# Kernel optimization log

Hardware: AMD Instinct MI355X
Metric: run time of the kernel (lower is better)

Reference implementation:

```python
import jax, jax.numpy as jnp
import numpy as np

D = 128  # input_dim

def setup_inputs() -> dict:
    key = jax.random.key(0)
    ks = jax.random.split(key, 9)
    B, Lq, Lkv = 4, 4096, 4096
    s = 1.0 / np.sqrt(D)
    return {
        "x1": jax.random.normal(ks[0], (B, Lq, D), dtype=jnp.float32),
        "x2": jax.random.normal(ks[1], (B, Lkv, D), dtype=jnp.float32),
        "x3": jax.random.normal(ks[2], (B, Lkv, D), dtype=jnp.float32),
        "Wq": jax.random.normal(ks[3], (D, D), dtype=jnp.float32) * s,
        "bq": jax.random.normal(ks[4], (D,), dtype=jnp.float32) * s,
        "Wk": jax.random.normal(ks[5], (D, D), dtype=jnp.float32) * s,
        "bk": jax.random.normal(ks[6], (D,), dtype=jnp.float32) * s,
        "Wv": jax.random.normal(ks[7], (D, D), dtype=jnp.float32) * s,
        "bv": jax.random.normal(ks[8], (D,), dtype=jnp.float32) * s,
    }

def reference(x1, x2, x3, Wq, bq, Wk, bk, Wv, bv):
    # torch Linear: y = x @ W.T + b
    q = jnp.einsum('bld,ed->ble', x1, Wq) + bq  # [B,Lq,D]
    k = jnp.einsum('bld,ed->ble', x2, Wk) + bk  # [B,Lkv,D]
    v = jnp.einsum('bld,ed->ble', x3, Wv) + bv  # [B,Lkv,D]
    scores = jnp.einsum('bqd,bkd->bqk', q, k) / jnp.sqrt(jnp.float32(x1.shape[-1]))
    attn = jax.nn.softmax(scores, axis=2)
    return jnp.einsum('bqk,bkd->bqd', attn, v)
```

## Files before the change

### kernel.cpp

```cpp
#include <hip/hip_runtime.h>
#include <hip/hip_bf16.h>

typedef __attribute__((ext_vector_type(8))) short short8;
typedef __attribute__((ext_vector_type(4))) float v4f;
typedef __attribute__((ext_vector_type(4))) unsigned int uint4v;

__device__ __forceinline__ unsigned short f2bf(float f) {
    union { float f; unsigned u; } c; c.f = f;
    unsigned r = c.u + 0x7FFFu + ((c.u >> 16) & 1u);
    return (unsigned short)(r >> 16);
}
__device__ __forceinline__ unsigned pack2(float a, float b) {
    return (unsigned)f2bf(a) | ((unsigned)f2bf(b) << 16);
}
__device__ __forceinline__ float bf2f(unsigned short h) {
    union { unsigned u; float f; } c; c.u = ((unsigned)h) << 16;
    return c.f;
}

__device__ __forceinline__ void g2l16(const unsigned short* g, unsigned short* l) {
    __builtin_amdgcn_global_load_lds(
        (const __attribute__((address_space(1))) unsigned int*)g,
        (__attribute__((address_space(3))) unsigned int*)l,
        16, 0, 0);
}

__global__ __launch_bounds__(512) void proj_kernel(
    const float* __restrict__ x1, const float* __restrict__ x2, const float* __restrict__ x3,
    const float* __restrict__ Wq, const float* __restrict__ bq,
    const float* __restrict__ Wk, const float* __restrict__ bk,
    const float* __restrict__ Wv, const float* __restrict__ bv,
    unsigned short* __restrict__ qb, unsigned short* __restrict__ kb,
    unsigned short* __restrict__ vb, float qscale)
{
    __shared__ __attribute__((aligned(16))) unsigned short Smem[32768];
    unsigned short* Xs = Smem;
    unsigned short* Ws = Smem + 16384;
    unsigned short* Os = Smem;

    int tid = threadIdx.x;
    int wave = tid >> 6, lane = tid & 63;
    int lmod = lane & 15, ldiv = lane >> 4;
    int p = blockIdx.x % 3;
    int row0 = (blockIdx.x / 3) * 128;

    const float* X = p == 0 ? x1 : p == 1 ? x2 : x3;
    const float* W = p == 0 ? Wq : p == 1 ? Wk : Wv;
    const float* bias = p == 0 ? bq : p == 1 ? bk : bv;
    float scale = p == 0 ? qscale : 1.0f;

#pragma unroll
    for (int i = 0; i < 8; i++) {
        int c = tid + i * 512;
        int row = c >> 5, d0 = (c & 31) * 4;
        v4f f = *(const v4f*)(X + (size_t)(row0 + row) * 128 + d0);
        int off = ((row >> 4) * 16 + (d0 >> 5) * 4 + ((d0 >> 3) & 3)) * 128 + (row & 15) * 8 + (d0 & 7);
        *(uint2*)&Xs[off] = make_uint2(pack2(f[0], f[1]), pack2(f[2], f[3]));
        v4f g = *(const v4f*)(W + (size_t)row * 128 + d0);
        *(uint2*)&Ws[off] = make_uint2(pack2(g[0], g[1]), pack2(g[2], g[3]));
    }
    __syncthreads();

    short8 af[4];
#pragma unroll
    for (int kc = 0; kc < 4; kc++)
        af[kc] = *(const short8*)&Xs[wave * 2048 + (kc * 4 + ldiv) * 128 + lmod * 8];
    __syncthreads();

#pragma unroll
    for (int ct = 0; ct < 8; ct++) {
        v4f acc = {0.f, 0.f, 0.f, 0.f};
#pragma unroll
        for (int kc = 0; kc < 4; kc++) {
            short8 bf = *(const short8*)&Ws[ct * 2048 + (kc * 4 + ldiv) * 128 + lmod * 8];
            acc = __builtin_amdgcn_mfma_f32_16x16x32_bf16(af[kc], bf, acc, 0, 0, 0);
        }
        int e = ct * 16 + lmod;
        float bv_ = bias[e];
#pragma unroll
        for (int r = 0; r < 4; r++) {
            int lrow = wave * 16 + ldiv * 4 + r;
            unsigned short h = f2bf((acc[r] + bv_) * scale);
            int off;
            if (p == 0) {
                off = lrow * 128 + e;
            } else if (p == 1) {
                int kk = lrow & 31, c = lrow >> 5;
                off = c * 4096 + (kk & 1) * 2048
                    + ((e >> 5) * 4 + ((e >> 3) & 3)) * 128 + (kk >> 1) * 8 + (e & 7);
            } else {
                int c = lrow >> 5;
                off = c * 4096 + ((e >> 4) * 4 + ((lrow >> 3) & 3)) * 128 + (e & 15) * 8 + (lrow & 7);
            }
            Os[off] = h;
        }
    }
    __syncthreads();

    unsigned short* dst;
    size_t gbase;
    if (p == 0) { dst = qb; gbase = (size_t)row0 * 128; }
    else {
        int b = row0 >> 12, key0 = row0 & 4095;
        gbase = (size_t)b * 524288 + (key0 >> 5) * 4096;
        dst = (p == 1) ? kb : vb;
    }
#pragma unroll
    for (int i = 0; i < 4; i++) {
        int c = (tid + i * 512) * 8;
        *(uint4v*)(dst + gbase + c) = *(const uint4v*)&Os[c];
    }
}

__global__ __launch_bounds__(256, 2) void attn_kernel(
    const unsigned short* __restrict__ Qb,
    const unsigned short* __restrict__ Kb,
    const unsigned short* __restrict__ Vb,
    unsigned short* __restrict__ Opart,
    float* __restrict__ Lbuf)
{
    __shared__ __attribute__((aligned(16))) unsigned short Smem[2 * 8192 + 2 * 8192 + 4 * 1280];
    unsigned short* KtB = Smem;
    unsigned short* VtB = Smem + 16384;
    unsigned short* PsB = Smem + 32768;

    int tid = threadIdx.x;
    int wave = tid >> 6, lane = tid & 63;
    int lmod = lane & 15, ldiv = lane >> 4;
    int qt = wave & 1, kg = wave >> 1;
    int split = blockIdx.x & 1;
    int rest = blockIdx.x >> 1;
    int b = rest >> 6;
    int q0 = (rest & 63) * 64 + qt * 32;

    short8 qfrag[2][4];
#pragma unroll
    for (int set = 0; set < 2; set++) {
        const unsigned short* qptr = Qb + (size_t)(b * 4096 + q0 + set * 16 + lmod) * 128;
#pragma unroll
        for (int kc = 0; kc < 4; kc++)
            qfrag[set][kc] = *(const short8*)(qptr + kc * 32 + ldiv * 8);
    }

    v4f oacc[2][8];
#pragma unroll
    for (int set = 0; set < 2; set++)
#pragma unroll
        for (int dt = 0; dt < 8; dt++) oacc[set][dt] = (v4f){0.f, 0.f, 0.f, 0.f};
    float lsum[2][4] = {{0.f, 0.f, 0.f, 0.f}, {0.f, 0.f, 0.f, 0.f}};

    const unsigned short* kbase = Kb + (size_t)b * 524288 + split * 262144;
    const unsigned short* vbase = Vb + (size_t)b * 524288 + split * 262144;

#pragma unroll
    for (int i = 0; i < 4; i++) {
        g2l16(kbase + wave * 2048 + i * 512 + lane * 8, &KtB[wave * 2048 + i * 512]);
        g2l16(vbase + wave * 2048 + i * 512 + lane * 8, &VtB[wave * 2048 + i * 512]);
    }
    __syncthreads();

    for (int t = 0; t < 32; t++) {
        int cur = t & 1;
        unsigned short* Kt = KtB + cur * 8192 + kg * 4096;
        unsigned short* Vt = VtB + cur * 8192 + kg * 4096;
        if (t < 31) {
            const unsigned short* kg_ = kbase + (t + 1) * 8192;
            const unsigned short* vg_ = vbase + (t + 1) * 8192;
            int nb = (cur ^ 1) * 8192;
#pragma unroll
            for (int i = 0; i < 4; i++) {
                g2l16(kg_ + wave * 2048 + i * 512 + lane * 8, &KtB[nb + wave * 2048 + i * 512]);
                g2l16(vg_ + wave * 2048 + i * 512 + lane * 8, &VtB[nb + wave * 2048 + i * 512]);
            }
        }

        v4f sacc[2][2];
#pragma unroll
        for (int set = 0; set < 2; set++)
#pragma unroll
            for (int s = 0; s < 2; s++) sacc[set][s] = (v4f){0.f, 0.f, 0.f, 0.f};
#pragma unroll
        for (int kc = 0; kc < 4; kc++) {
            short8 kf0 = *(const short8*)&Kt[(kc * 4 + ldiv) * 128 + lmod * 8];
            short8 kf1 = *(const short8*)&Kt[2048 + (kc * 4 + ldiv) * 128 + lmod * 8];
            sacc[0][0] = __builtin_amdgcn_mfma_f32_16x16x32_bf16(qfrag[0][kc], kf0, sacc[0][0], 0, 0, 0);
            sacc[0][1] = __builtin_amdgcn_mfma_f32_16x16x32_bf16(qfrag[0][kc], kf1, sacc[0][1], 0, 0, 0);
            sacc[1][0] = __builtin_amdgcn_mfma_f32_16x16x32_bf16(qfrag[1][kc], kf0, sacc[1][0], 0, 0, 0);
            sacc[1][1] = __builtin_amdgcn_mfma_f32_16x16x32_bf16(qfrag[1][kc], kf1, sacc[1][1], 0, 0, 0);
        }

        unsigned short* Ps = PsB + wave * 1280;
#pragma unroll
        for (int set = 0; set < 2; set++)
#pragma unroll
            for (int r = 0; r < 4; r++) {
                float p0 = __builtin_amdgcn_exp2f(sacc[set][0][r]);
                float p1 = __builtin_amdgcn_exp2f(sacc[set][1][r]);
                lsum[set][r] += p0 + p1;
                *(unsigned*)&Ps[(set * 16 + 4 * ldiv + r) * 40 + lmod * 2] = pack2(p0, p1);
            }
        asm volatile("s_waitcnt lgkmcnt(0)" ::: "memory");

        short8 pf0 = *(const short8*)&Ps[lmod * 40 + ldiv * 8];
        short8 pf1 = *(const short8*)&Ps[(16 + lmod) * 40 + ldiv * 8];
#pragma unroll
        for (int dt = 0; dt < 8; dt++) {
            short8 vf = *(const short8*)&Vt[(dt * 4 + ldiv) * 128 + lmod * 8];
            oacc[0][dt] = __builtin_amdgcn_mfma_f32_16x16x32_bf16(pf0, vf, oacc[0][dt], 0, 0, 0);
            oacc[1][dt] = __builtin_amdgcn_mfma_f32_16x16x32_bf16(pf1, vf, oacc[1][dt], 0, 0, 0);
        }
        __syncthreads();
    }

    float lred[2][4];
#pragma unroll
    for (int set = 0; set < 2; set++)
#pragma unroll
        for (int r = 0; r < 4; r++) {
            float lv = lsum[set][r];
            lv += __shfl_xor(lv, 1);
            lv += __shfl_xor(lv, 2);
            lv += __shfl_xor(lv, 4);
            lv += __shfl_xor(lv, 8);
            lred[set][r] = lv;
        }

    float* Obuf = (float*)Smem;
    float* Lb2  = (float*)PsB;
    if (kg == 1) {
#pragma unroll
        for (int set = 0; set < 2; set++)
#pragma unroll
            for (int r = 0; r < 4; r++) {
                int row = qt * 32 + set * 16 + 4 * ldiv + r;
#pragma unroll
                for (int dt = 0; dt < 8; dt++)
                    Obuf[row * 130 + dt * 16 + lmod] = oacc[set][dt][r];
                if (lmod == 0) Lb2[row] = lred[set][r];
            }
    }
    __syncthreads();
    if (kg == 0) {
#pragma unroll
        for (int set = 0; set < 2; set++)
#pragma unroll
            for (int r = 0; r < 4; r++) {
                int row = qt * 32 + set * 16 + 4 * ldiv + r;
                int gq = b * 4096 + q0 + set * 16 + 4 * ldiv + r;
                if (lmod == 0) Lbuf[split * 16384 + gq] = lred[set][r] + Lb2[row];
                unsigned short* obase = Opart + (size_t)(split * 16384 + gq) * 128;
#pragma unroll
                for (int dt = 0; dt < 8; dt++)
                    obase[dt * 16 + lmod] = f2bf(oacc[set][dt][r] + Obuf[row * 130 + dt * 16 + lmod]);
            }
    }
}

__global__ __launch_bounds__(256) void merge_kernel(
    const unsigned short* __restrict__ Opart,
    const float* __restrict__ Lbuf,
    float* __restrict__ Out)
{
    int t = blockIdx.x * 256 + threadIdx.x;
#pragma unroll
    for (int it = 0; it < 4; it++) {
        int base = (t + it * 65536) * 8;
        int q = base >> 7;
        float inv = 1.0f / (Lbuf[q] + Lbuf[16384 + q]);
        short8 o0 = *(const short8*)(Opart + base);
        short8 o1 = *(const short8*)(Opart + 2097152 + base);
        float acc[8];
#pragma unroll
        for (int j = 0; j < 8; j++)
            acc[j] = (bf2f((unsigned short)o0[j]) + bf2f((unsigned short)o1[j])) * inv;
        *(v4f*)(Out + base) = (v4f){acc[0], acc[1], acc[2], acc[3]};
        *(v4f*)(Out + base + 4) = (v4f){acc[4], acc[5], acc[6], acc[7]};
    }
}

extern "C" void kernel_launch(void* const* d_in, const int* in_sizes, int n_in,
                              void* d_out, int out_size, void* d_ws, size_t ws_size,
                              hipStream_t stream) {
    const float* x1 = (const float*)d_in[0];
    const float* x2 = (const float*)d_in[1];
    const float* x3 = (const float*)d_in[2];
    const float* Wq = (const float*)d_in[3];
    const float* bq = (const float*)d_in[4];
    const float* Wk = (const float*)d_in[5];
    const float* bk = (const float*)d_in[6];
    const float* Wv = (const float*)d_in[7];
    const float* bv = (const float*)d_in[8];
    float* out = (float*)d_out;

    unsigned short* qb = (unsigned short*)d_ws;
    unsigned short* kb = qb + (size_t)2097152;
    unsigned short* vb = kb + (size_t)2097152;
    unsigned short* op = vb + (size_t)2097152;
    float* lb = (float*)(op + (size_t)4194304);

    const float qscale = 1.4426950408889634f / 11.313708498984761f;

    proj_kernel<<<384, 512, 0, stream>>>(x1, x2, x3, Wq, bq, Wk, bk, Wv, bv,
                                         qb, kb, vb, qscale);
    attn_kernel<<<512, 256, 0, stream>>>(qb, kb, vb, op, lb);
    merge_kernel<<<256, 256, 0, stream>>>(op, lb, out);
}
```

Baseline: 142.7 us.

## Split KV eight ways, widen per-wave query tile, use 32x32 MFMA for PV

The attention kernel now splits the KV sequence into 8 chunks per block group, with each wave owning 64 query rows against a 32-key tile. The PV product switches to 32x32x16 MFMA, which needs a new V layout written by the projection kernel. This removes the in-block cross-wave reduction through shared memory and improves K/V reuse across more query rows per wave. In exchange, the partial outputs written to workspace grow fourfold and the merge kernel must read and sum eight partials, which adds memory traffic.

After: 155.7 us. +9.1%, slower.

```diff
diff --git a/kernel.cpp b/kernel.cpp
--- a/kernel.cpp
+++ b/kernel.cpp
@@ -3,6 +3,7 @@
 
 typedef __attribute__((ext_vector_type(8))) short short8;
 typedef __attribute__((ext_vector_type(4))) float v4f;
+typedef __attribute__((ext_vector_type(16))) float v16f;
 typedef __attribute__((ext_vector_type(4))) unsigned int uint4v;
 
 __device__ __forceinline__ unsigned short f2bf(float f) {
@@ -17,7 +18,6 @@
     union { unsigned u; float f; } c; c.u = ((unsigned)h) << 16;
     return c.f;
 }
-
 __device__ __forceinline__ void g2l16(const unsigned short* g, unsigned short* l) {
     __builtin_amdgcn_global_load_lds(
         (const __attribute__((address_space(1))) unsigned int*)g,
@@ -89,8 +89,9 @@
                 off = c * 4096 + (kk & 1) * 2048
                     + ((e >> 5) * 4 + ((e >> 3) & 3)) * 128 + (kk >> 1) * 8 + (e & 7);
             } else {
-                int c = lrow >> 5;
-                off = c * 4096 + ((e >> 4) * 4 + ((lrow >> 3) & 3)) * 128 + (e & 15) * 8 + (lrow & 7);
+                int kk = lrow & 31, c = lrow >> 5;
+                off = c * 4096 + (kk >> 4) * 2048 + (e >> 5) * 512
+                    + (e & 31) * 16 + ((kk >> 3) & 1) * 8 + (kk & 7);
             }
             Os[off] = h;
         }
@@ -119,141 +120,128 @@
     unsigned short* __restrict__ Opart,
     float* __restrict__ Lbuf)
 {
-    __shared__ __attribute__((aligned(16))) unsigned short Smem[2 * 8192 + 2 * 8192 + 4 * 1280];
-    unsigned short* KtB = Smem;
-    unsigned short* VtB = Smem + 16384;
-    unsigned short* PsB = Smem + 32768;
+    __shared__ __attribute__((aligned(16))) unsigned short KtB[2][4096];
+    __shared__ __attribute__((aligned(16))) unsigned short VtB[2][4096];
+    __shared__ __attribute__((aligned(16))) unsigned short PsB[4][2560];
 
     int tid = threadIdx.x;
     int wave = tid >> 6, lane = tid & 63;
     int lmod = lane & 15, ldiv = lane >> 4;
-    int qt = wave & 1, kg = wave >> 1;
-    int split = blockIdx.x & 1;
-    int rest = blockIdx.x >> 1;
-    int b = rest >> 6;
-    int q0 = (rest & 63) * 64 + qt * 32;
-
-    short8 qfrag[2][4];
-#pragma unroll
-    for (int set = 0; set < 2; set++) {
-        const unsigned short* qptr = Qb + (size_t)(b * 4096 + q0 + set * 16 + lmod) * 128;
+    int l5 = lane & 31, lh = lane >> 5;
+    int split = blockIdx.x & 7;
+    int qg = blockIdx.x >> 3;
+    int b = qg >> 4;
+    int q0 = (qg & 15) * 256 + wave * 64;
+
+    short8 qfrag[4][4];
+#pragma unroll
+    for (int s4 = 0; s4 < 4; s4++) {
+        const unsigned short* qptr = Qb + (size_t)(b * 4096 + q0 + s4 * 16 + lmod) * 128;
 #pragma unroll
         for (int kc = 0; kc < 4; kc++)
-            qfrag[set][kc] = *(const short8*)(qptr + kc * 32 + ldiv * 8);
-    }
-
-    v4f oacc[2][8];
-#pragma unroll
-    for (int set = 0; set < 2; set++)
-#pragma unroll
-        for (int dt = 0; dt < 8; dt++) oacc[set][dt] = (v4f){0.f, 0.f, 0.f, 0.f};
-    float lsum[2][4] = {{0.f, 0.f, 0.f, 0.f}, {0.f, 0.f, 0.f, 0.f}};
-
-    const unsigned short* kbase = Kb + (size_t)b * 524288 + split * 262144;
-    const unsigned short* vbase = Vb + (size_t)b * 524288 + split * 262144;
-
-#pragma unroll
-    for (int i = 0; i < 4; i++) {
-        g2l16(kbase + wave * 2048 + i * 512 + lane * 8, &KtB[wave * 2048 + i * 512]);
-        g2l16(vbase + wave * 2048 + i * 512 + lane * 8, &VtB[wave * 2048 + i * 512]);
-    }
-    __syncthreads();
-
-    for (int t = 0; t < 32; t++) {
+            qfrag[s4][kc] = *(const short8*)(qptr + kc * 32 + ldiv * 8);
+    }
+
+    v16f oacc[2][4];
+#pragma unroll
+    for (int qt = 0; qt < 2; qt++)
+#pragma unroll
+        for (int nt = 0; nt < 4; nt++)
+#pragma unroll
+            for (int i = 0; i < 16; i++) oacc[qt][nt][i] = 0.f;
+    float lsum[4][4] = {{0.f}, {0.f}, {0.f}, {0.f}};
+
+    const unsigned short* kbase = Kb + (size_t)b * 524288 + split * 65536;
+    const unsigned short* vbase = Vb + (size_t)b * 524288 + split * 65536;
+
+#pragma unroll
+    for (int i = 0; i < 2; i++) {
+        g2l16(kbase + wave * 1024 + i * 512 + lane * 8, &KtB[0][wave * 1024 + i * 512]);
+        g2l16(vbase + wave * 1024 + i * 512 + lane * 8, &VtB[0][wave * 1024 + i * 512]);
+    }
+    __syncthreads();
+
+    for (int t = 0; t < 16; t++) {
         int cur = t & 1;
-        unsigned short* Kt = KtB + cur * 8192 + kg * 4096;
-        unsigned short* Vt = VtB + cur * 8192 + kg * 4096;
-        if (t < 31) {
-            const unsigned short* kg_ = kbase + (t + 1) * 8192;
-            const unsigned short* vg_ = vbase + (t + 1) * 8192;
-            int nb = (cur ^ 1) * 8192;
-#pragma unroll
-            for (int i = 0; i < 4; i++) {
-                g2l16(kg_ + wave * 2048 + i * 512 + lane * 8, &KtB[nb + wave * 2048 + i * 512]);
-                g2l16(vg_ + wave * 2048 + i * 512 + lane * 8, &VtB[nb + wave * 2048 + i * 512]);
-            }
-        }
-
-        v4f sacc[2][2];
-#pragma unroll
-        for (int set = 0; set < 2; set++)
-#pragma unroll
-            for (int s = 0; s < 2; s++) sacc[set][s] = (v4f){0.f, 0.f, 0.f, 0.f};
+        const unsigned short* Kt = KtB[cur];
+        const unsigned short* Vt = VtB[cur];
+        if (t < 15) {
+            const unsigned short* kg = kbase + (t + 1) * 4096;
+            const unsigned short* vg = vbase + (t + 1) * 4096;
+#pragma unroll
+            for (int i = 0; i < 2; i++) {
+                g2l16(kg + wave * 1024 + i * 512 + lane * 8, &KtB[cur ^ 1][wave * 1024 + i * 512]);
+                g2l16(vg + wave * 1024 + i * 512 + lane * 8, &VtB[cur ^ 1][wave * 1024 + i * 512]);
+            }
+        }
+
+        v4f sacc[4][2];
+#pragma unroll
+        for (int s4 = 0; s4 < 4; s4++)
+#pragma unroll
+            for (int s = 0; s < 2; s++) sacc[s4][s] = (v4f){0.f, 0.f, 0.f, 0.f};
 #pragma unroll
         for (int kc = 0; kc < 4; kc++) {
             short8 kf0 = *(const short8*)&Kt[(kc * 4 + ldiv) * 128 + lmod * 8];
             short8 kf1 = *(const short8*)&Kt[2048 + (kc * 4 + ldiv) * 128 + lmod * 8];
-            sacc[0][0] = __builtin_amdgcn_mfma_f32_16x16x32_bf16(qfrag[0][kc], kf0, sacc[0][0], 0, 0, 0);
-            sacc[0][1] = __builtin_amdgcn_mfma_f32_16x16x32_bf16(qfrag[0][kc], kf1, sacc[0][1], 0, 0, 0);
-            sacc[1][0] = __builtin_amdgcn_mfma_f32_16x16x32_bf16(qfrag[1][kc], kf0, sacc[1][0], 0, 0, 0);
-            sacc[1][1] = __builtin_amdgcn_mfma_f32_16x16x32_bf16(qfrag[1][kc], kf1, sacc[1][1], 0, 0, 0);
-        }
-
-        unsigned short* Ps = PsB + wave * 1280;
-#pragma unroll
-        for (int set = 0; set < 2; set++)
+#pragma unroll
+            for (int s4 = 0; s4 < 4; s4++) {
+                sacc[s4][0] = __builtin_amdgcn_mfma_f32_16x16x32_bf16(qfrag[s4][kc], kf0, sacc[s4][0], 0, 0, 0);
+                sacc[s4][1] = __builtin_amdgcn_mfma_f32_16x16x32_bf16(qfrag[s4][kc], kf1, sacc[s4][1], 0, 0, 0);
+            }
+        }
+
+        unsigned short* Ps = PsB[wave];
+#pragma unroll
+        for (int s4 = 0; s4 < 4; s4++)
 #pragma unroll
             for (int r = 0; r < 4; r++) {
-                float p0 = __builtin_amdgcn_exp2f(sacc[set][0][r]);
-                float p1 = __builtin_amdgcn_exp2f(sacc[set][1][r]);
-                lsum[set][r] += p0 + p1;
-                *(unsigned*)&Ps[(set * 16 + 4 * ldiv + r) * 40 + lmod * 2] = pack2(p0, p1);
+                float p0 = __builtin_amdgcn_exp2f(sacc[s4][0][r]);
+                float p1 = __builtin_amdgcn_exp2f(sacc[s4][1][r]);
+                lsum[s4][r] += p0 + p1;
+                *(unsigned*)&Ps[(s4 * 16 + ldiv * 4 + r) * 40 + lmod * 2] = pack2(p0, p1);
             }
         asm volatile("s_waitcnt lgkmcnt(0)" ::: "memory");
 
-        short8 pf0 = *(const short8*)&Ps[lmod * 40 + ldiv * 8];
-        short8 pf1 = *(const short8*)&Ps[(16 + lmod) * 40 + ldiv * 8];
-#pragma unroll
-        for (int dt = 0; dt < 8; dt++) {
-            short8 vf = *(const short8*)&Vt[(dt * 4 + ldiv) * 128 + lmod * 8];
-            oacc[0][dt] = __builtin_amdgcn_mfma_f32_16x16x32_bf16(pf0, vf, oacc[0][dt], 0, 0, 0);
-            oacc[1][dt] = __builtin_amdgcn_mfma_f32_16x16x32_bf16(pf1, vf, oacc[1][dt], 0, 0, 0);
+#pragma unroll
+        for (int kc2 = 0; kc2 < 2; kc2++) {
+            short8 pf0 = *(const short8*)&Ps[l5 * 40 + kc2 * 16 + lh * 8];
+            short8 pf1 = *(const short8*)&Ps[(32 + l5) * 40 + kc2 * 16 + lh * 8];
+#pragma unroll
+            for (int nt = 0; nt < 4; nt++) {
+                short8 vf = *(const short8*)&Vt[kc2 * 2048 + nt * 512 + l5 * 16 + lh * 8];
+                oacc[0][nt] = __builtin_amdgcn_mfma_f32_32x32x16_bf16(pf0, vf, oacc[0][nt], 0, 0, 0);
+                oacc[1][nt] = __builtin_amdgcn_mfma_f32_32x32x16_bf16(pf1, vf, oacc[1][nt], 0, 0, 0);
+            }
         }
         __syncthreads();
     }
 
-    float lred[2][4];
-#pragma unroll
-    for (int set = 0; set < 2; set++)
+#pragma unroll
+    for (int s4 = 0; s4 < 4; s4++)
 #pragma unroll
         for (int r = 0; r < 4; r++) {
-            float lv = lsum[set][r];
+            float lv = lsum[s4][r];
             lv += __shfl_xor(lv, 1);
             lv += __shfl_xor(lv, 2);
             lv += __shfl_xor(lv, 4);
             lv += __shfl_xor(lv, 8);
-            lred[set][r] = lv;
-        }
-
-    float* Obuf = (float*)Smem;
-    float* Lb2  = (float*)PsB;
-    if (kg == 1) {
-#pragma unroll
-        for (int set = 0; set < 2; set++)
-#pragma unroll
-            for (int r = 0; r < 4; r++) {
-                int row = qt * 32 + set * 16 + 4 * ldiv + r;
-#pragma unroll
-                for (int dt = 0; dt < 8; dt++)
-                    Obuf[row * 130 + dt * 16 + lmod] = oacc[set][dt][r];
-                if (lmod == 0) Lb2[row] = lred[set][r];
-            }
-    }
-    __syncthreads();
-    if (kg == 0) {
-#pragma unroll
-        for (int set = 0; set < 2; set++)
-#pragma unroll
-            for (int r = 0; r < 4; r++) {
-                int row = qt * 32 + set * 16 + 4 * ldiv + r;
-                int gq = b * 4096 + q0 + set * 16 + 4 * ldiv + r;
-                if (lmod == 0) Lbuf[split * 16384 + gq] = lred[set][r] + Lb2[row];
-                unsigned short* obase = Opart + (size_t)(split * 16384 + gq) * 128;
-#pragma unroll
-                for (int dt = 0; dt < 8; dt++)
-                    obase[dt * 16 + lmod] = f2bf(oacc[set][dt][r] + Obuf[row * 130 + dt * 16 + lmod]);
-            }
-    }
+            if (lmod == 0) {
+                int gq = b * 4096 + q0 + s4 * 16 + ldiv * 4 + r;
+                Lbuf[split * 16384 + gq] = lv;
+            }
+        }
+
+#pragma unroll
+    for (int qt = 0; qt < 2; qt++)
+#pragma unroll
+        for (int nt = 0; nt < 4; nt++)
+#pragma unroll
+            for (int i = 0; i < 16; i++) {
+                int qrow = qt * 32 + (i & 3) + 8 * (i >> 2) + 4 * lh;
+                int gq = b * 4096 + q0 + qrow;
+                Opart[((size_t)split * 16384 + gq) * 128 + nt * 32 + l5] = f2bf(oacc[qt][nt][i]);
+            }
 }
 
 __global__ __launch_bounds__(256) void merge_kernel(
@@ -266,15 +254,19 @@
     for (int it = 0; it < 4; it++) {
         int base = (t + it * 65536) * 8;
         int q = base >> 7;
-        float inv = 1.0f / (Lbuf[q] + Lbuf[16384 + q]);
-        short8 o0 = *(const short8*)(Opart + base);
-        short8 o1 = *(const short8*)(Opart + 2097152 + base);
-        float acc[8];
-#pragma unroll
-        for (int j = 0; j < 8; j++)
-            acc[j] = (bf2f((unsigned short)o0[j]) + bf2f((unsigned short)o1[j])) * inv;
-        *(v4f*)(Out + base) = (v4f){acc[0], acc[1], acc[2], acc[3]};
-        *(v4f*)(Out + base + 4) = (v4f){acc[4], acc[5], acc[6], acc[7]};
+        float lt = 0.f;
+#pragma unroll
+        for (int s = 0; s < 8; s++) lt += Lbuf[s * 16384 + q];
+        float inv = 1.0f / lt;
+        float acc[8] = {0.f, 0.f, 0.f, 0.f, 0.f, 0.f, 0.f, 0.f};
+#pragma unroll
+        for (int s = 0; s < 8; s++) {
+            short8 o = *(const short8*)(Opart + (size_t)s * 2097152 + base);
+#pragma unroll
+            for (int j = 0; j < 8; j++) acc[j] += bf2f((unsigned short)o[j]);
+        }
+        *(v4f*)(Out + base) = (v4f){acc[0] * inv, acc[1] * inv, acc[2] * inv, acc[3] * inv};
+        *(v4f*)(Out + base + 4) = (v4f){acc[4] * inv, acc[5] * inv, acc[6] * inv, acc[7] * inv};
     }
 }
 
@@ -296,7 +288,7 @@
     unsigned short* kb = qb + (size_t)2097152;
     unsigned short* vb = kb + (size_t)2097152;
     unsigned short* op = vb + (size_t)2097152;
-    float* lb = (float*)(op + (size_t)4194304);
+    float* lb = (float*)(op + (size_t)16777216);
 
     const float qscale = 1.4426950408889634f / 11.313708498984761f;
 
```
